# Optimization experiments

Hardware: AMD Instinct MI355X
Metric: run time of the kernel (lower is better)

Reference implementation:

```python
import math
import jax, jax.numpy as jnp
import numpy as np

B, S, DIM = 1, 2048, 2048
N_HEADS, N_KV_HEADS = 32, 8
HEAD_DIM = DIM // N_HEADS  # 64
HIDDEN = 8192  # 4*dim, already a multiple of 256
EPS = 1e-5


def setup_inputs() -> dict:
    key = jax.random.key(0)
    ks = jax.random.split(key, 10)

    def xavier(k, shape):
        lim = math.sqrt(6.0 / (shape[0] + shape[1]))
        return jax.random.uniform(k, shape, jnp.float32, -lim, lim)

    x = jax.random.normal(ks[0], (B, S, DIM), jnp.float32)
    c = jax.random.normal(ks[1], (B, DIM), jnp.float32)
    x_mask = jnp.ones((B, S), dtype=bool)
    # RoPE angles (theta=10000), freqs_cis = exp(i * pos * inv_freq) -> cos/sin parts
    inv_freq = 1.0 / (10000.0 ** (jnp.arange(0, HEAD_DIM, 2, dtype=jnp.float32) / HEAD_DIM))
    ang = jnp.arange(S, dtype=jnp.float32)[:, None] * inv_freq[None, :]  # [S, HEAD_DIM//2]
    freqs_cos = jnp.broadcast_to(jnp.cos(ang)[None], (B, S, HEAD_DIM // 2))
    freqs_sin = jnp.broadcast_to(jnp.sin(ang)[None], (B, S, HEAD_DIM // 2))
    qkv_out = (N_HEADS + 2 * N_KV_HEADS) * HEAD_DIM
    return dict(
        x=x, x_mask=x_mask, freqs_cos=freqs_cos, freqs_sin=freqs_sin, c=c,
        w_qkv=xavier(ks[2], (qkv_out, DIM)),
        w_out=xavier(ks[3], (DIM, N_HEADS * HEAD_DIM)),
        q_norm_w=jnp.ones((HEAD_DIM,), jnp.float32),
        k_norm_w=jnp.ones((HEAD_DIM,), jnp.float32),
        attn_norm1_w=jnp.ones((DIM,), jnp.float32),
        attn_norm2_w=jnp.ones((DIM,), jnp.float32),
        ffn_norm1_w=jnp.ones((DIM,), jnp.float32),
        ffn_norm2_w=jnp.ones((DIM,), jnp.float32),
        w1=xavier(ks[4], (HIDDEN, DIM)),
        w2=xavier(ks[5], (DIM, HIDDEN)),
        w3=xavier(ks[6], (HIDDEN, DIM)),
        w_ada=0.02 * jax.random.normal(ks[7], (4 * DIM, DIM), jnp.float32),
        b_ada=jnp.zeros((4 * DIM,), jnp.float32),
    )


def rms_norm(x, w, eps=EPS):
    x32 = x.astype(jnp.float32)
    return (x32 * jax.lax.rsqrt(jnp.mean(x32 * x32, -1, keepdims=True) + eps)).astype(x.dtype) * w


def apply_rope(x, cos, sin):
    # x: [b,s,h,d]; complex pairing of consecutive elements (view_as_complex)
    xr, xi = x[..., 0::2], x[..., 1::2]
    c = cos[:, :, None, :]  # broadcast over heads (freqs_cis.unsqueeze(2))
    s = sin[:, :, None, :]
    return jnp.stack([xr * c - xi * s, xr * s + xi * c], axis=-1).reshape(x.shape)


def reference(x, x_mask, freqs_cos, freqs_sin, c, w_qkv, w_out, q_norm_w, k_norm_w,
              attn_norm1_w, attn_norm2_w, ffn_norm1_w, ffn_norm2_w, w1, w2, w3,
              w_ada, b_ada):
    b, s, _ = x.shape
    n_rep = N_HEADS // N_KV_HEADS
    # AdaLN modulation: SiLU -> Linear -> 4 chunks
    mod = jax.nn.silu(c) @ w_ada.T + b_ada                      # [b, 4*dim]
    scale_msa, gate_msa, scale_mlp, gate_mlp = jnp.split(mod, 4, axis=-1)
    # ---- attention branch ----
    h = rms_norm(x, attn_norm1_w) * (1.0 + scale_msa[:, None, :])
    qkv = h @ w_qkv.T
    q, k, v = jnp.split(qkv, [N_HEADS * HEAD_DIM, (N_HEADS + N_KV_HEADS) * HEAD_DIM], axis=-1)
    q = q.reshape(b, s, N_HEADS, HEAD_DIM)
    k = k.reshape(b, s, N_KV_HEADS, HEAD_DIM)
    v = v.reshape(b, s, N_KV_HEADS, HEAD_DIM)
    q = rms_norm(q, q_norm_w)
    k = rms_norm(k, k_norm_w)
    q = apply_rope(q, freqs_cos, freqs_sin)
    k = apply_rope(k, freqs_cos, freqs_sin)
    # GQA: repeat each kv head n_rep times consecutively (unsqueeze+repeat+flatten)
    k = jnp.repeat(k, n_rep, axis=2)
    v = jnp.repeat(v, n_rep, axis=2)
    scale = math.sqrt(1.0 / HEAD_DIM)
    scores = jnp.einsum('bqhd,bkhd->bhqk', q, k) * scale         # [b,H,s,s]
    scores = jnp.where(x_mask[:, None, None, :], scores, -1e30)
    probs = jax.nn.softmax(scores, axis=-1)
    attn = jnp.einsum('bhqk,bkhd->bqhd', probs, v).reshape(b, s, N_HEADS * HEAD_DIM)
    attn = attn @ w_out.T
    x = x + jnp.tanh(gate_msa)[:, None, :] * rms_norm(attn, attn_norm2_w)
    # ---- SwiGLU FFN branch ----
    h = rms_norm(x, ffn_norm1_w) * (1.0 + scale_mlp[:, None, :])
    ffn = (jax.nn.silu(h @ w1.T) * (h @ w3.T)) @ w2.T
    x = x + jnp.tanh(gate_mlp)[:, None, :] * rms_norm(ffn, ffn_norm2_w)
    return x
```

## Files before the change

### kernel.cpp

```cpp
#include <hip/hip_runtime.h>
#include <hip/hip_bf16.h>
#include <cstdint>

typedef __hip_bfloat16 bf16;
typedef __attribute__((ext_vector_type(8))) short s8v;
typedef __attribute__((ext_vector_type(4))) float f32x4;

#define MFMA_BF16(a,b,c) __builtin_amdgcn_mfma_f32_16x16x32_bf16((a),(b),(c),0,0,0)

__device__ __forceinline__ float bf2f(bf16 v) { return __bfloat162float(v); }
__device__ __forceinline__ bf16 f2bf(float v) { return __float2bfloat16(v); }
__device__ __forceinline__ short f2bfbits(float v) {
  bf16 b = __float2bfloat16(v);
  short s; __builtin_memcpy(&s, &b, 2); return s;
}
__device__ __forceinline__ void g2lds16(const void* g, void* l) {
  __builtin_amdgcn_global_load_lds((__attribute__((address_space(1))) void*)(g),
                                   (__attribute__((address_space(3))) void*)(l), 16, 0, 0);
}
__device__ __forceinline__ void load8(const bf16* p, float v[8]) {
  uint4 r = *reinterpret_cast<const uint4*>(p);
  v[0]=__uint_as_float(r.x<<16); v[1]=__uint_as_float(r.x&0xffff0000u);
  v[2]=__uint_as_float(r.y<<16); v[3]=__uint_as_float(r.y&0xffff0000u);
  v[4]=__uint_as_float(r.z<<16); v[5]=__uint_as_float(r.z&0xffff0000u);
  v[6]=__uint_as_float(r.w<<16); v[7]=__uint_as_float(r.w&0xffff0000u);
}
__device__ __forceinline__ void loadf8(const float* p, float v[8]) {
  float4 a = *(const float4*)p, b = *(const float4*)(p + 4);
  v[0]=a.x; v[1]=a.y; v[2]=a.z; v[3]=a.w;
  v[4]=b.x; v[5]=b.y; v[6]=b.z; v[7]=b.w;
}
__device__ __forceinline__ s8v cvt8(const float* p) {
  float4 a = *(const float4*)p, b = *(const float4*)(p + 4);
  s8v r;
  r[0]=f2bfbits(a.x); r[1]=f2bfbits(a.y); r[2]=f2bfbits(a.z); r[3]=f2bfbits(a.w);
  r[4]=f2bfbits(b.x); r[5]=f2bfbits(b.y); r[6]=f2bfbits(b.z); r[7]=f2bfbits(b.w);
  return r;
}

__global__ __launch_bounds__(256) void ndt_cvt(
    const float* __restrict__ s, bf16* __restrict__ d, long n) {
  long i = ((long)blockIdx.x * 256 + threadIdx.x) * 8;
  if (i >= n) return;
  *(s8v*)(d + i) = cvt8(s + i);
}

__global__ __launch_bounds__(256) void ndt_ada(
    const float* __restrict__ c, const float* __restrict__ w_ada,
    const float* __restrict__ b_ada, float* __restrict__ mods) {
  const int wave = threadIdx.x >> 6, lane = threadIdx.x & 63;
  const int out = blockIdx.x * 4 + wave;
  const float4* wrow = (const float4*)(w_ada + (long)out * 2048);
  const float4* c4 = (const float4*)c;
  float acc = 0.f;
  for (int k = lane; k < 512; k += 64) {
    float4 wv = wrow[k];
    float4 cv = c4[k];
    acc += (cv.x / (1.f + __expf(-cv.x))) * wv.x;
    acc += (cv.y / (1.f + __expf(-cv.y))) * wv.y;
    acc += (cv.z / (1.f + __expf(-cv.z))) * wv.z;
    acc += (cv.w / (1.f + __expf(-cv.w))) * wv.w;
  }
  #pragma unroll
  for (int o = 32; o; o >>= 1) acc += __shfl_xor(acc, o, 64);
  if (lane == 0) {
    float m = acc + b_ada[out];
    int grp = out >> 11, idx = out & 2047;
    mods[grp * 2048 + idx] = (grp & 1) ? tanhf(m) : (1.f + m);
  }
}

__global__ __launch_bounds__(256) void ndt_norm_mod(
    const float* __restrict__ x, const float* __restrict__ w,
    const float* __restrict__ smod, bf16* __restrict__ out) {
  const int t = blockIdx.x, tid = threadIdx.x;
  __shared__ float red[4];
  float v[8];
  loadf8(x + (long)t * 2048 + tid * 8, v);
  float ss = 0.f;
  #pragma unroll
  for (int i = 0; i < 8; i++) ss += v[i] * v[i];
  #pragma unroll
  for (int o = 32; o; o >>= 1) ss += __shfl_xor(ss, o, 64);
  if ((tid & 63) == 0) red[tid >> 6] = ss;
  __syncthreads();
  float r = rsqrtf((red[0]+red[1]+red[2]+red[3]) * (1.f/2048.f) + 1e-5f);
  #pragma unroll
  for (int i = 0; i < 8; i++) {
    int cc = tid * 8 + i;
    out[(long)t * 2048 + cc] = f2bf(v[i] * r * w[cc] * smod[cc]);
  }
}

template<int EPI>
__global__ __launch_bounds__(256) void ndt_gemm_bb(
    const bf16* __restrict__ A, const bf16* __restrict__ B,
    bf16* __restrict__ C, const bf16* __restrict__ aux,
    int M, int N, int K) {
  __shared__ alignas(16) short sA[128 * 32];
  __shared__ alignas(16) short sB[128 * 32];
  const int tid = threadIdx.x;
  const int wave = tid >> 6, lane = tid & 63;
  const int quad = lane >> 4, l15 = lane & 15;
  const int wm = (wave >> 1) << 6, wn = (wave & 1) << 6;
  const long m0 = (long)blockIdx.x * 128, n0 = (long)blockIdx.y * 128;
  f32x4 zero4 = {0.f, 0.f, 0.f, 0.f};
  f32x4 acc[4][4];
  #pragma unroll
  for (int i = 0; i < 4; i++)
    #pragma unroll
    for (int j = 0; j < 4; j++) acc[i][j] = zero4;
  const int srow = lane >> 2;
  const int skc  = (lane & 3) * 8;
  for (int k0 = 0; k0 < K; k0 += 32) {
    #pragma unroll
    for (int it = 0; it < 2; it++) {
      int seg = wave * 2 + it;
      int row = seg * 16 + srow;
      g2lds16(A + (m0 + row) * (long)K + k0 + skc, (char*)sA + seg * 1024);
      g2lds16(B + (n0 + row) * (long)K + k0 + skc, (char*)sB + seg * 1024);
    }
    __syncthreads();
    s8v af[4], bfr[4];
    #pragma unroll
    for (int i = 0; i < 4; i++) af[i]  = *(const s8v*)&sA[(wm + i*16 + l15)*32 + quad*8];
    #pragma unroll
    for (int j = 0; j < 4; j++) bfr[j] = *(const s8v*)&sB[(wn + j*16 + l15)*32 + quad*8];
    #pragma unroll
    for (int i = 0; i < 4; i++)
      #pragma unroll
      for (int j = 0; j < 4; j++)
        acc[i][j] = MFMA_BF16(af[i], bfr[j], acc[i][j]);
    __syncthreads();
  }
  #pragma unroll
  for (int i = 0; i < 4; i++) {
    long rg = m0 + wm + i*16 + quad*4;
    #pragma unroll
    for (int j = 0; j < 4; j++) {
      long cg = n0 + wn + j*16 + l15;
      #pragma unroll
      for (int r = 0; r < 4; r++) {
        float v = acc[i][j][r];
        long idx = (rg + r) * (long)N + cg;
        if (EPI == 1) v = v / (1.f + __expf(-v));
        if (EPI == 2) v = v * bf2f(aux[idx]);
        C[idx] = f2bf(v);
      }
    }
  }
}

__device__ __forceinline__ void stage64(const bf16* __restrict__ G, long g0,
                                        int K, int t, char* tile, int q, int tid) {
  int L = q * 8192 + tid * 16;
  int Ls = L ^ (((L >> 9) & 1) << 5);
  const char* src = (const char*)(G + (g0 + (Ls >> 7)) * (long)K + t * 64) + (Ls & 127);
  g2lds16(src, tile + L);
}

__device__ __forceinline__ void phase_bar() {
  asm volatile("" ::: "memory");
  __builtin_amdgcn_s_barrier();
  asm volatile("" ::: "memory");
}

#define READ_A8(tA, h) do { \
  _Pragma("unroll") for (int i_ = 0; i_ < 4; i_++) { \
    int row_ = wm * 128 + (h) * 64 + i_ * 16 + l15; \
    _Pragma("unroll") for (int kk_ = 0; kk_ < 2; kk_++) { \
      int P_ = row_ * 128 + kk_ * 64 + quad * 16; \
      af[kk_][i_] = *(const s8v*)((tA) + (P_ ^ (((P_ >> 9) & 1) << 5))); } } } while (0)

#define READ_B8(tB, nh, bfreg) do { \
  _Pragma("unroll") for (int j_ = 0; j_ < 2; j_++) { \
    int col_ = wn * 64 + (nh) * 32 + j_ * 16 + l15; \
    _Pragma("unroll") for (int kk_ = 0; kk_ < 2; kk_++) { \
      int P_ = col_ * 128 + kk_ * 64 + quad * 16; \
      bfreg[kk_][j_] = *(const s8v*)((tB) + (P_ ^ (((P_ >> 9) & 1) << 5))); } } } while (0)

#define MMQ8(h, nh, bfreg) do { \
  __builtin_amdgcn_s_setprio(1); \
  _Pragma("unroll") for (int i_ = 0; i_ < 4; i_++) \
    _Pragma("unroll") for (int j_ = 0; j_ < 2; j_++) { \
      acc[(h)*4 + i_][(nh)*2 + j_] = MFMA_BF16(af[0][i_], bfreg[0][j_], acc[(h)*4 + i_][(nh)*2 + j_]); \
      acc[(h)*4 + i_][(nh)*2 + j_] = MFMA_BF16(af[1][i_], bfreg[1][j_], acc[(h)*4 + i_][(nh)*2 + j_]); } \
  __builtin_amdgcn_s_setprio(0); } while (0)

template<int EPI>
__global__ __launch_bounds__(512, 2) void ndt_gemm8(
    const bf16* __restrict__ A, const bf16* __restrict__ B,
    bf16* __restrict__ C, const bf16* __restrict__ aux,
    int M, int N, int K) {
  __shared__ alignas(16) short lds8[65536];
  char* const tA0 = (char*)lds8;
  char* const tB0 = tA0 + 32768;
  char* const tA1 = tA0 + 65536;
  char* const tB1 = tA0 + 98304;

  const int tid = threadIdx.x;
  const int wid = tid >> 6, lane = tid & 63;
  const int quad = lane >> 4, l15 = lane & 15;
  const int wm = wid >> 2, wn = wid & 3;

  const int nbx = gridDim.x;
  int bid = blockIdx.y * nbx + blockIdx.x;
  const int nwg = nbx * (int)gridDim.y;
  if ((nwg & 7) == 0) bid = (bid & 7) * (nwg >> 3) + (bid >> 3);
  const long m0 = (long)(bid % nbx) * 256;
  const long n0 = (long)(bid / nbx) * 256;

  const int NT = K >> 6;
  const int NI = NT >> 1;

  f32x4 acc[8][4];
  f32x4 zero4 = {0.f, 0.f, 0.f, 0.f};
  #pragma unroll
  for (int i = 0; i < 8; i++)
    #pragma unroll
    for (int j = 0; j < 4; j++) acc[i][j] = zero4;

  s8v af[2][4], bf0[2][2], bf1[2][2];

  #pragma unroll
  for (int q = 0; q < 4; q++) stage64(A, m0, K, 0, tA0, q, tid);
  #pragma unroll
  for (int q = 0; q < 4; q++) stage64(B, n0, K, 0, tB0, q, tid);
  #pragma unroll
  for (int q = 0; q < 4; q++) stage64(A, m0, K, 1, tA1, q, tid);
  stage64(B, n0, K, 1, tB1, 0, tid);
  stage64(B, n0, K, 1, tB1, 1, tid);
  asm volatile("s_waitcnt vmcnt(6)" ::: "memory");
  phase_bar();

  for (int it = 0; it < NI; ++it) {
    const int T = 2 * it;
    const int t2 = (T + 2 < NT) ? T + 2 : NT - 1;
    const int t3 = (T + 3 < NT) ? T + 3 : NT - 1;
    READ_A8(tA0, 0);
    READ_B8(tB0, 0, bf0);
    stage64(B, n0, K, T + 1, tB1, 2, tid);
    stage64(B, n0, K, T + 1, tB1, 3, tid);
    phase_bar(); MMQ8(0, 0, bf0); phase_bar();
    READ_B8(tB0, 1, bf1);
    stage64(A, m0, K, t2, tA0, 0, tid);
    stage64(A, m0, K, t2, tA0, 2, tid);
    phase_bar(); MMQ8(0, 1, bf1); phase_bar();
    READ_A8(tA0, 1);
    stage64(B, n0, K, t2, tB0, 0, tid);
    stage64(B, n0, K, t2, tB0, 1, tid);
    phase_bar(); MMQ8(1, 0, bf0); phase_bar();
    stage64(A, m0, K, t2, tA0, 1, tid);
    stage64(A, m0, K, t2, tA0, 3, tid);
    asm volatile("s_waitcnt vmcnt(6)" ::: "memory");
    phase_bar(); MMQ8(1, 1, bf1); phase_bar();
    READ_A8(tA1, 0);
    READ_B8(tB1, 0, bf0);
    stage64(B, n0, K, t2, tB0, 2, tid);
    stage64(B, n0, K, t2, tB0, 3, tid);
    phase_bar(); MMQ8(0, 0, bf0); phase_bar();
    READ_B8(tB1, 1, bf1);
    stage64(A, m0, K, t3, tA1, 0, tid);
    stage64(A, m0, K, t3, tA1, 2, tid);
    phase_bar(); MMQ8(0, 1, bf1); phase_bar();
    READ_A8(tA1, 1);
    stage64(B, n0, K, t3, tB1, 0, tid);
    stage64(B, n0, K, t3, tB1, 1, tid);
    phase_bar(); MMQ8(1, 0, bf0); phase_bar();
    stage64(A, m0, K, t3, tA1, 1, tid);
    stage64(A, m0, K, t3, tA1, 3, tid);
    asm volatile("s_waitcnt vmcnt(6)" ::: "memory");
    phase_bar(); MMQ8(1, 1, bf1); phase_bar();
  }
  asm volatile("s_waitcnt vmcnt(0)" ::: "memory");

  #pragma unroll
  for (int mi = 0; mi < 8; mi++) {
    long rg = m0 + wm * 128 + mi * 16 + quad * 4;
    #pragma unroll
    for (int nj = 0; nj < 4; nj++) {
      long cg = n0 + wn * 64 + nj * 16 + l15;
      #pragma unroll
      for (int r = 0; r < 4; r++) {
        float v = acc[mi][nj][r];
        long idx = (rg + r) * (long)N + cg;
        if (EPI == 1) v = v / (1.f + __expf(-v));
        if (EPI == 2) v = v * bf2f(aux[idx]);
        C[idx] = f2bf(v);
      }
    }
  }
}

template<int EPI>
__global__ __launch_bounds__(256) void ndt_gemm_bt(
    const bf16* __restrict__ A, const float* __restrict__ B,
    bf16* __restrict__ C, const bf16* __restrict__ aux,
    int M, int N, int K) {
  __shared__ alignas(16) short sA[128 * 32];
  __shared__ alignas(16) short sB[128 * 32];
  const int tid = threadIdx.x;
  const int wave = tid >> 6, lane = tid & 63;
  const int quad = lane >> 4, l15 = lane & 15;
  const int wm = (wave >> 1) << 6, wn = (wave & 1) << 6;
  const long m0 = (long)blockIdx.x * 128, n0 = (long)blockIdx.y * 128;
  f32x4 zero4 = {0.f, 0.f, 0.f, 0.f};
  f32x4 acc[4][4];
  #pragma unroll
  for (int i = 0; i < 4; i++)
    #pragma unroll
    for (int j = 0; j < 4; j++) acc[i][j] = zero4;
  const int srow = lane >> 2;
  const int skc  = (lane & 3) * 8;
  const int r0 = (wave * 2) * 16 + srow;
  const int r1 = (wave * 2 + 1) * 16 + srow;
  const bf16*  pa0 = A + (m0 + r0) * (long)K + skc;
  const bf16*  pa1 = A + (m0 + r1) * (long)K + skc;
  const float* pb0 = B + (n0 + r0) * (long)K + skc;
  const float* pb1 = B + (n0 + r1) * (long)K + skc;
  uint4* da0 = (uint4*)&sA[r0 * 32 + skc];
  uint4* da1 = (uint4*)&sA[r1 * 32 + skc];
  s8v* db0 = (s8v*)&sB[r0 * 32 + skc];
  s8v* db1 = (s8v*)&sB[r1 * 32 + skc];
  for (int k0 = 0; k0 < K; k0 += 32) {
    uint4 va0 = *(const uint4*)pa0; pa0 += 32;
    uint4 va1 = *(const uint4*)pa1; pa1 += 32;
    s8v vb0 = cvt8(pb0); pb0 += 32;
    s8v vb1 = cvt8(pb1); pb1 += 32;
    *da0 = va0; *da1 = va1; *db0 = vb0; *db1 = vb1;
    __syncthreads();
    s8v af[4], bfr[4];
    #pragma unroll
    for (int i = 0; i < 4; i++) af[i]  = *(const s8v*)&sA[(wm + i*16 + l15)*32 + quad*8];
    #pragma unroll
    for (int j = 0; j < 4; j++) bfr[j] = *(const s8v*)&sB[(wn + j*16 + l15)*32 + quad*8];
    #pragma unroll
    for (int i = 0; i < 4; i++)
      #pragma unroll
      for (int j = 0; j < 4; j++)
        acc[i][j] = MFMA_BF16(af[i], bfr[j], acc[i][j]);
    __syncthreads();
  }
  #pragma unroll
  for (int i = 0; i < 4; i++) {
    long rg = m0 + wm + i*16 + quad*4;
    #pragma unroll
    for (int j = 0; j < 4; j++) {
      long cg = n0 + wn + j*16 + l15;
      #pragma unroll
      for (int r = 0; r < 4; r++) {
        float v = acc[i][j][r];
        long idx = (rg + r) * (long)N + cg;
        if (EPI == 1) v = v / (1.f + __expf(-v));
        if (EPI == 2) v = v * bf2f(aux[idx]);
        C[idx] = f2bf(v);
      }
    }
  }
}

__global__ __launch_bounds__(256) void ndt_qkrope(
    const bf16* __restrict__ qkv, const float* __restrict__ qw, const float* __restrict__ kw,
    const float* __restrict__ fc, const float* __restrict__ fs,
    bf16* __restrict__ qb, bf16* __restrict__ kb, bf16* __restrict__ vb) {
  const int wid = blockIdx.x * 4 + (threadIdx.x >> 6);
  const int lane = threadIdx.x & 63;
  const int t = wid / 48;
  const int u = wid - t * 48;
  if (u < 40) {
    const bool isq = (u < 32);
    const int hh = isq ? u : (u - 32);
    const long src = (long)t * 3072 + (isq ? hh * 64 : 2048 + hh * 64) + lane;
    float v = bf2f(qkv[src]);
    float ss = v * v;
    #pragma unroll
    for (int o = 32; o; o >>= 1) ss += __shfl_xor(ss, o, 64);
    float r = rsqrtf(ss * (1.f/64.f) + 1e-5f);
    float y = v * r * (isq ? qw[lane] : kw[lane]);
    int j = lane >> 1;
    float cv = fc[t * 32 + j];
    float sv = fs[t * 32 + j];
    float p = __shfl_xor(y, 1, 64);
    float out = (lane & 1) ? (p * sv + y * cv) : (y * cv - p * sv);
    if (isq) qb[(long)t * 2048 + hh * 64 + lane] = f2bf(out);
    else     kb[(long)t * 512 + hh * 64 + lane] = f2bf(out);
  } else {
    const int vh = u - 40;
    vb[(long)t * 512 + vh * 64 + lane] = qkv[(long)t * 3072 + 2560 + vh * 64 + lane];
  }
}

__global__ __launch_bounds__(256) void ndt_attn(
    const bf16* __restrict__ qb, const bf16* __restrict__ kb,
    const bf16* __restrict__ vb, bf16* __restrict__ ob) {
  const int h = blockIdx.y;
  const int qblk = blockIdx.x;
  const int tid = threadIdx.x;
  const int wave = tid >> 6, lane = tid & 63;
  const int quad = lane >> 4, l15 = lane & 15;
  const int kh = h >> 2;
  __shared__ alignas(16) short kT[64 * 72];
  __shared__ alignas(16) short vT[64 * 72];
  __shared__ alignas(16) short pT[4][16 * 72];
  const int qrow = qblk * 64 + wave * 16 + l15;
  const short* qptr = (const short*)qb + (long)qrow * 2048 + h * 64;
  s8v qf0 = *(const s8v*)(qptr + quad * 8);
  s8v qf1 = *(const s8v*)(qptr + 32 + quad * 8);
  f32x4 zero4 = {0.f, 0.f, 0.f, 0.f};
  f32x4 o[4];
  float mr[4], lr[4];
  #pragma unroll
  for (int r = 0; r < 4; r++) { o[r] = zero4; mr[r] = -1e30f; lr[r] = 0.f; }
  const int skey = tid >> 2;
  const int sdg = (tid & 3) * 16;
  for (int kt = 0; kt < 32; kt++) {
    {
      const short* ksrc = (const short*)kb + ((long)(kt * 64 + skey) * 8 + kh) * 64 + sdg;
      *(uint4*)&kT[skey * 72 + sdg]     = *(const uint4*)(ksrc);
      *(uint4*)&kT[skey * 72 + sdg + 8] = *(const uint4*)(ksrc + 8);
      const short* vsrc = (const short*)vb + ((long)(kt * 64 + skey) * 8 + kh) * 64 + sdg;
      short tv[16];
      *(uint4*)&tv[0] = *(const uint4*)(vsrc);
      *(uint4*)&tv[8] = *(const uint4*)(vsrc + 8);
      #pragma unroll
      for (int i = 0; i < 16; i++) vT[(sdg + i) * 72 + skey] = tv[i];
    }
    __syncthreads();
    f32x4 s[4];
    #pragma unroll
    for (int b4 = 0; b4 < 4; b4++) {
      const short* kr = &kT[(b4 * 16 + l15) * 72];
      s8v kf0 = *(const s8v*)(kr + quad * 8);
      s8v kf1 = *(const s8v*)(kr + 32 + quad * 8);
      f32x4 z = zero4;
      z = MFMA_BF16(qf0, kf0, z);
      z = MFMA_BF16(qf1, kf1, z);
      s[b4] = z;
    }
    #pragma unroll
    for (int r = 0; r < 4; r++) {
      float mx = -1e30f;
      #pragma unroll
      for (int b4 = 0; b4 < 4; b4++) { float sv2 = s[b4][r] * 0.125f; s[b4][r] = sv2; mx = fmaxf(mx, sv2); }
      mx = fmaxf(mx, __shfl_xor(mx, 1, 64));
      mx = fmaxf(mx, __shfl_xor(mx, 2, 64));
      mx = fmaxf(mx, __shfl_xor(mx, 4, 64));
      mx = fmaxf(mx, __shfl_xor(mx, 8, 64));
      float nm = fmaxf(mr[r], mx);
      float alpha = __expf(mr[r] - nm);
      mr[r] = nm;
      float rs = 0.f;
      #pragma unroll
      for (int b4 = 0; b4 < 4; b4++) { float p = __expf(s[b4][r] - nm); s[b4][r] = p; rs += p; }
      rs += __shfl_xor(rs, 1, 64);
      rs += __shfl_xor(rs, 2, 64);
      rs += __shfl_xor(rs, 4, 64);
      rs += __shfl_xor(rs, 8, 64);
      lr[r] = lr[r] * alpha + rs;
      #pragma unroll
      for (int cb = 0; cb < 4; cb++) o[cb][r] *= alpha;
    }
    short* pw = &pT[wave][0];
    #pragma unroll
    for (int b4 = 0; b4 < 4; b4++)
      #pragma unroll
      for (int r = 0; r < 4; r++)
        pw[(quad * 4 + r) * 72 + b4 * 16 + l15] = f2bfbits(s[b4][r]);
    const short* pr = &pT[wave][0];
    s8v pf0 = *(const s8v*)(pr + l15 * 72 + quad * 8);
    s8v pf1 = *(const s8v*)(pr + l15 * 72 + 32 + quad * 8);
    #pragma unroll
    for (int cb = 0; cb < 4; cb++) {
      const short* vr = &vT[(cb * 16 + l15) * 72];
      s8v vf0 = *(const s8v*)(vr + quad * 8);
      s8v vf1 = *(const s8v*)(vr + 32 + quad * 8);
      o[cb] = MFMA_BF16(pf0, vf0, o[cb]);
      o[cb] = MFMA_BF16(pf1, vf1, o[cb]);
    }
    __syncthreads();
  }
  #pragma unroll
  for (int cb = 0; cb < 4; cb++)
    #pragma unroll
    for (int r = 0; r < 4; r++) {
      int tok = qblk * 64 + wave * 16 + quad * 4 + r;
      ob[(long)tok * 2048 + h * 64 + cb * 16 + l15] = f2bf(o[cb][r] / lr[r]);
    }
}

__global__ __launch_bounds__(256) void ndt_resid1(
    const float* __restrict__ x, const bf16* __restrict__ ao,
    const float* __restrict__ mods, const float* __restrict__ w_n2,
    const float* __restrict__ w_f1, float* __restrict__ x1, bf16* __restrict__ h2) {
  const int t = blockIdx.x, tid = threadIdx.x;
  __shared__ float red1[4], red2[4];
  const long base = (long)t * 2048;
  float a[8], xv[8], y[8];
  load8(ao + base + tid * 8, a);
  loadf8(x + base + tid * 8, xv);
  float ss = 0.f;
  #pragma unroll
  for (int i = 0; i < 8; i++) ss += a[i] * a[i];
  #pragma unroll
  for (int o = 32; o; o >>= 1) ss += __shfl_xor(ss, o, 64);
  if ((tid & 63) == 0) red1[tid >> 6] = ss;
  __syncthreads();
  float r1 = rsqrtf((red1[0]+red1[1]+red1[2]+red1[3]) * (1.f/2048.f) + 1e-5f);
  float ss2 = 0.f;
  #pragma unroll
  for (int i = 0; i < 8; i++) {
    int cc = tid * 8 + i;
    float yy = xv[i] + mods[2048 + cc] * (a[i] * r1 * w_n2[cc]);
    y[i] = yy; ss2 += yy * yy;
    x1[base + cc] = yy;
  }
  #pragma unroll
  for (int o = 32; o; o >>= 1) ss2 += __shfl_xor(ss2, o, 64);
  if ((tid & 63) == 0) red2[tid >> 6] = ss2;
  __syncthreads();
  float r2 = rsqrtf((red2[0]+red2[1]+red2[2]+red2[3]) * (1.f/2048.f) + 1e-5f);
  #pragma unroll
  for (int i = 0; i < 8; i++) {
    int cc = tid * 8 + i;
    h2[base + cc] = f2bf(y[i] * r2 * w_f1[cc] * mods[4096 + cc]);
  }
}

__global__ __launch_bounds__(256) void ndt_resid2(
    const float* __restrict__ x1, const bf16* __restrict__ ffn,
    const float* __restrict__ mods, const float* __restrict__ w_f2,
    float* __restrict__ out) {
  const int t = blockIdx.x, tid = threadIdx.x;
  __shared__ float red[4];
  const long base = (long)t * 2048;
  float f[8], xv[8];
  load8(ffn + base + tid * 8, f);
  loadf8(x1 + base + tid * 8, xv);
  float ss = 0.f;
  #pragma unroll
  for (int i = 0; i < 8; i++) ss += f[i] * f[i];
  #pragma unroll
  for (int o = 32; o; o >>= 1) ss += __shfl_xor(ss, o, 64);
  if ((tid & 63) == 0) red[tid >> 6] = ss;
  __syncthreads();
  float r = rsqrtf((red[0]+red[1]+red[2]+red[3]) * (1.f/2048.f) + 1e-5f);
  #pragma unroll
  for (int i = 0; i < 8; i++) {
    int cc = tid * 8 + i;
    out[base + cc] = xv[i] + mods[6144 + cc] * (f[i] * r * w_f2[cc]);
  }
}

extern "C" void kernel_launch(void* const* d_in, const int* in_sizes, int n_in,
                              void* d_out, int out_size, void* d_ws, size_t ws_size,
                              hipStream_t stream) {
  const float* x     = (const float*)d_in[0];
  const float* fc    = (const float*)d_in[2];
  const float* fs    = (const float*)d_in[3];
  const float* c     = (const float*)d_in[4];
  const float* w_qkv = (const float*)d_in[5];
  const float* w_out = (const float*)d_in[6];
  const float* q_nw  = (const float*)d_in[7];
  const float* k_nw  = (const float*)d_in[8];
  const float* an1   = (const float*)d_in[9];
  const float* an2   = (const float*)d_in[10];
  const float* fn1   = (const float*)d_in[11];
  const float* fn2   = (const float*)d_in[12];
  const float* w1    = (const float*)d_in[13];
  const float* w2    = (const float*)d_in[14];
  const float* w3    = (const float*)d_in[15];
  const float* w_ada = (const float*)d_in[16];
  const float* b_ada = (const float*)d_in[17];
  float* out = (float*)d_out;

  const size_t MB = 1024 * 1024;
  char* w = (char*)d_ws;
  float* mods = (float*)(w);
  char* base = w + 32768;
  bf16* h1   = (bf16*)(base);
  bf16* attn = h1;
  bf16* ffn  = h1;
  bf16* qkv  = (bf16*)(base + 8 * MB);
  bf16* ao   = qkv;
  bf16* qb   = (bf16*)(base + 20 * MB);
  bf16* h2   = qb;
  bf16* kb   = (bf16*)(base + 28 * MB);
  bf16* vb   = (bf16*)(base + 30 * MB);
  float* x1  = (float*)(base + 32 * MB);
  bf16* t1   = (bf16*)(base + 48 * MB);
  bf16* Wa   = (bf16*)(base + 80 * MB);
  bf16* Wb   = (bf16*)(base + 112 * MB);
  const size_t needed = 32768 + 144 * MB;

  ndt_ada<<<2048, 256, 0, stream>>>(c, w_ada, b_ada, mods);
  ndt_norm_mod<<<2048, 256, 0, stream>>>(x, an1, mods, h1);

  if (ws_size >= needed) {
    ndt_cvt<<<3072, 256, 0, stream>>>(w_qkv, Wa, 6291456L);
    ndt_gemm_bb<0><<<dim3(16, 24), 256, 0, stream>>>(h1, Wa, qkv, nullptr, 2048, 3072, 2048);
    ndt_qkrope<<<24576, 256, 0, stream>>>(qkv, q_nw, k_nw, fc, fs, qb, kb, vb);
    ndt_attn<<<dim3(32, 32), 256, 0, stream>>>(qb, kb, vb, attn);
    ndt_cvt<<<2048, 256, 0, stream>>>(w_out, Wa, 4194304L);
    ndt_gemm_bb<0><<<dim3(16, 16), 256, 0, stream>>>(attn, Wa, ao, nullptr, 2048, 2048, 2048);
    ndt_resid1<<<2048, 256, 0, stream>>>(x, ao, mods, an2, fn1, x1, h2);
    ndt_cvt<<<8192, 256, 0, stream>>>(w1, Wa, 16777216L);
    ndt_cvt<<<8192, 256, 0, stream>>>(w3, Wb, 16777216L);
    ndt_gemm8<1><<<dim3(8, 32), 512, 0, stream>>>(h2, Wa, t1, nullptr, 2048, 8192, 2048);
    ndt_gemm8<2><<<dim3(8, 32), 512, 0, stream>>>(h2, Wb, t1, t1, 2048, 8192, 2048);
    ndt_cvt<<<8192, 256, 0, stream>>>(w2, Wa, 16777216L);
    ndt_gemm_bb<0><<<dim3(16, 16), 256, 0, stream>>>(t1, Wa, ffn, nullptr, 2048, 2048, 8192);
  } else {
    ndt_gemm_bt<0><<<dim3(16, 24), 256, 0, stream>>>(h1, w_qkv, qkv, nullptr, 2048, 3072, 2048);
    ndt_qkrope<<<24576, 256, 0, stream>>>(qkv, q_nw, k_nw, fc, fs, qb, kb, vb);
    ndt_attn<<<dim3(32, 32), 256, 0, stream>>>(qb, kb, vb, attn);
    ndt_gemm_bt<0><<<dim3(16, 16), 256, 0, stream>>>(attn, w_out, ao, nullptr, 2048, 2048, 2048);
    ndt_resid1<<<2048, 256, 0, stream>>>(x, ao, mods, an2, fn1, x1, h2);
    ndt_gemm_bt<1><<<dim3(16, 64), 256, 0, stream>>>(h2, w1, t1, nullptr, 2048, 8192, 2048);
    ndt_gemm_bt<2><<<dim3(16, 64), 256, 0, stream>>>(h2, w3, t1, t1, 2048, 8192, 2048);
    ndt_gemm_bt<0><<<dim3(16, 16), 256, 0, stream>>>(t1, w2, ffn, nullptr, 2048, 2048, 8192);
  }
  ndt_resid2<<<2048, 256, 0, stream>>>(x1, ffn, mods, fn2, out);
}
```

Measured before the change: 893.1 us.

## Use split-K 256x256 GEMM for QKV, out-proj and down-proj with fp32 partials

Replaces the simple 128x128 GEMM used for the QKV, output-projection and FFN down-projection with the pipelined 256x256 kernel. Because those GEMMs have few output tiles, K is split across blockIdx.z and the fp32 partial sums go to workspace buffers. The partials are added up inside new fused epilogue kernels for qk-norm/rope, residual1 and residual2. It also changes the LDS swizzle and precomputes staging source pointers. The cost is extra fp32 partial traffic through global memory and more reads in the epilogue kernels.

```diff
diff --git a/kernel.cpp b/kernel.cpp
--- a/kernel.cpp
+++ b/kernel.cpp
@@ -92,106 +92,45 @@
   }
 }
 
-template<int EPI>
-__global__ __launch_bounds__(256) void ndt_gemm_bb(
-    const bf16* __restrict__ A, const bf16* __restrict__ B,
-    bf16* __restrict__ C, const bf16* __restrict__ aux,
-    int M, int N, int K) {
-  __shared__ alignas(16) short sA[128 * 32];
-  __shared__ alignas(16) short sB[128 * 32];
-  const int tid = threadIdx.x;
-  const int wave = tid >> 6, lane = tid & 63;
-  const int quad = lane >> 4, l15 = lane & 15;
-  const int wm = (wave >> 1) << 6, wn = (wave & 1) << 6;
-  const long m0 = (long)blockIdx.x * 128, n0 = (long)blockIdx.y * 128;
-  f32x4 zero4 = {0.f, 0.f, 0.f, 0.f};
-  f32x4 acc[4][4];
-  #pragma unroll
-  for (int i = 0; i < 4; i++)
-    #pragma unroll
-    for (int j = 0; j < 4; j++) acc[i][j] = zero4;
-  const int srow = lane >> 2;
-  const int skc  = (lane & 3) * 8;
-  for (int k0 = 0; k0 < K; k0 += 32) {
-    #pragma unroll
-    for (int it = 0; it < 2; it++) {
-      int seg = wave * 2 + it;
-      int row = seg * 16 + srow;
-      g2lds16(A + (m0 + row) * (long)K + k0 + skc, (char*)sA + seg * 1024);
-      g2lds16(B + (n0 + row) * (long)K + k0 + skc, (char*)sB + seg * 1024);
-    }
-    __syncthreads();
-    s8v af[4], bfr[4];
-    #pragma unroll
-    for (int i = 0; i < 4; i++) af[i]  = *(const s8v*)&sA[(wm + i*16 + l15)*32 + quad*8];
-    #pragma unroll
-    for (int j = 0; j < 4; j++) bfr[j] = *(const s8v*)&sB[(wn + j*16 + l15)*32 + quad*8];
-    #pragma unroll
-    for (int i = 0; i < 4; i++)
-      #pragma unroll
-      for (int j = 0; j < 4; j++)
-        acc[i][j] = MFMA_BF16(af[i], bfr[j], acc[i][j]);
-    __syncthreads();
-  }
-  #pragma unroll
-  for (int i = 0; i < 4; i++) {
-    long rg = m0 + wm + i*16 + quad*4;
-    #pragma unroll
-    for (int j = 0; j < 4; j++) {
-      long cg = n0 + wn + j*16 + l15;
-      #pragma unroll
-      for (int r = 0; r < 4; r++) {
-        float v = acc[i][j][r];
-        long idx = (rg + r) * (long)N + cg;
-        if (EPI == 1) v = v / (1.f + __expf(-v));
-        if (EPI == 2) v = v * bf2f(aux[idx]);
-        C[idx] = f2bf(v);
-      }
-    }
-  }
-}
-
-__device__ __forceinline__ void stage64(const bf16* __restrict__ G, long g0,
-                                        int K, int t, char* tile, int q, int tid) {
-  int L = q * 8192 + tid * 16;
-  int Ls = L ^ (((L >> 9) & 1) << 5);
-  const char* src = (const char*)(G + (g0 + (Ls >> 7)) * (long)K + t * 64) + (Ls & 127);
-  g2lds16(src, tile + L);
-}
-
-__device__ __forceinline__ void phase_bar() {
-  asm volatile("" ::: "memory");
-  __builtin_amdgcn_s_barrier();
-  asm volatile("" ::: "memory");
-}
+#define SWZ8(P) ((P) ^ ((((P) >> 7) & 7) << 4))
+
+#define STG8(mat, q, t, tile) \
+  g2lds16(src##mat[q] + (long)(t) * 128, (tile) + (q) * 8192 + (tid << 4))
 
 #define READ_A8(tA, h) do { \
   _Pragma("unroll") for (int i_ = 0; i_ < 4; i_++) { \
     int row_ = wm * 128 + (h) * 64 + i_ * 16 + l15; \
     _Pragma("unroll") for (int kk_ = 0; kk_ < 2; kk_++) { \
       int P_ = row_ * 128 + kk_ * 64 + quad * 16; \
-      af[kk_][i_] = *(const s8v*)((tA) + (P_ ^ (((P_ >> 9) & 1) << 5))); } } } while (0)
+      af[kk_][i_] = *(const s8v*)((tA) + SWZ8(P_)); } } } while (0)
 
 #define READ_B8(tB, nh, bfreg) do { \
   _Pragma("unroll") for (int j_ = 0; j_ < 2; j_++) { \
     int col_ = wn * 64 + (nh) * 32 + j_ * 16 + l15; \
     _Pragma("unroll") for (int kk_ = 0; kk_ < 2; kk_++) { \
       int P_ = col_ * 128 + kk_ * 64 + quad * 16; \
-      bfreg[kk_][j_] = *(const s8v*)((tB) + (P_ ^ (((P_ >> 9) & 1) << 5))); } } } while (0)
-
-#define MMQ8(h, nh, bfreg) do { \
+      bfreg[kk_][j_] = *(const s8v*)((tB) + SWZ8(P_)); } } } while (0)
+
+#define PH_MMA(h, nh, bfreg) do { \
+  asm volatile("" ::: "memory"); \
+  __builtin_amdgcn_s_barrier(); \
+  asm volatile("s_waitcnt lgkmcnt(0)" ::: "memory"); \
+  __builtin_amdgcn_sched_barrier(0); \
   __builtin_amdgcn_s_setprio(1); \
   _Pragma("unroll") for (int i_ = 0; i_ < 4; i_++) \
     _Pragma("unroll") for (int j_ = 0; j_ < 2; j_++) { \
       acc[(h)*4 + i_][(nh)*2 + j_] = MFMA_BF16(af[0][i_], bfreg[0][j_], acc[(h)*4 + i_][(nh)*2 + j_]); \
       acc[(h)*4 + i_][(nh)*2 + j_] = MFMA_BF16(af[1][i_], bfreg[1][j_], acc[(h)*4 + i_][(nh)*2 + j_]); } \
-  __builtin_amdgcn_s_setprio(0); } while (0)
-
-template<int EPI>
+  __builtin_amdgcn_s_setprio(0); \
+  asm volatile("" ::: "memory"); \
+  __builtin_amdgcn_s_barrier(); \
+  asm volatile("" ::: "memory"); } while (0)
+
+template<int EPI, int SPLIT>
 __global__ __launch_bounds__(512, 2) void ndt_gemm8(
     const bf16* __restrict__ A, const bf16* __restrict__ B,
-    bf16* __restrict__ C, const bf16* __restrict__ aux,
-    int M, int N, int K) {
+    void* __restrict__ C0, void* __restrict__ C1, const bf16* __restrict__ aux,
+    int M, int N, int ldK, int Kc) {
   __shared__ alignas(16) short lds8[65536];
   char* const tA0 = (char*)lds8;
   char* const tB0 = tA0 + 32768;
@@ -209,9 +148,20 @@
   if ((nwg & 7) == 0) bid = (bid & 7) * (nwg >> 3) + (bid >> 3);
   const long m0 = (long)(bid % nbx) * 256;
   const long n0 = (long)(bid / nbx) * 256;
-
-  const int NT = K >> 6;
+  const long koff = (long)blockIdx.z * Kc;
+
+  const int NT = Kc >> 6;
   const int NI = NT >> 1;
+
+  const char* srcA[4];
+  const char* srcB[4];
+  #pragma unroll
+  for (int q = 0; q < 4; q++) {
+    int L = q * 8192 + (tid << 4);
+    int Ls = SWZ8(L);
+    srcA[q] = (const char*)(A + (m0 + (Ls >> 7)) * (long)ldK + koff) + (Ls & 127);
+    srcB[q] = (const char*)(B + (n0 + (Ls >> 7)) * (long)ldK + koff) + (Ls & 127);
+  }
 
   f32x4 acc[8][4];
   f32x4 zero4 = {0.f, 0.f, 0.f, 0.f};
@@ -223,15 +173,17 @@
   s8v af[2][4], bf0[2][2], bf1[2][2];
 
   #pragma unroll
-  for (int q = 0; q < 4; q++) stage64(A, m0, K, 0, tA0, q, tid);
-  #pragma unroll
-  for (int q = 0; q < 4; q++) stage64(B, n0, K, 0, tB0, q, tid);
-  #pragma unroll
-  for (int q = 0; q < 4; q++) stage64(A, m0, K, 1, tA1, q, tid);
-  stage64(B, n0, K, 1, tB1, 0, tid);
-  stage64(B, n0, K, 1, tB1, 1, tid);
+  for (int q = 0; q < 4; q++) STG8(A, q, 0, tA0);
+  #pragma unroll
+  for (int q = 0; q < 4; q++) STG8(B, q, 0, tB0);
+  #pragma unroll
+  for (int q = 0; q < 4; q++) STG8(A, q, 1, tA1);
+  STG8(B, 0, 1, tB1);
+  STG8(B, 1, 1, tB1);
   asm volatile("s_waitcnt vmcnt(6)" ::: "memory");
-  phase_bar();
+  asm volatile("" ::: "memory");
+  __builtin_amdgcn_s_barrier();
+  asm volatile("" ::: "memory");
 
   for (int it = 0; it < NI; ++it) {
     const int T = 2 * it;
@@ -239,54 +191,71 @@
     const int t3 = (T + 3 < NT) ? T + 3 : NT - 1;
     READ_A8(tA0, 0);
     READ_B8(tB0, 0, bf0);
-    stage64(B, n0, K, T + 1, tB1, 2, tid);
-    stage64(B, n0, K, T + 1, tB1, 3, tid);
-    phase_bar(); MMQ8(0, 0, bf0); phase_bar();
+    STG8(B, 2, T + 1, tB1);
+    STG8(B, 3, T + 1, tB1);
+    PH_MMA(0, 0, bf0);
     READ_B8(tB0, 1, bf1);
-    stage64(A, m0, K, t2, tA0, 0, tid);
-    stage64(A, m0, K, t2, tA0, 2, tid);
-    phase_bar(); MMQ8(0, 1, bf1); phase_bar();
+    STG8(A, 0, t2, tA0);
+    STG8(A, 2, t2, tA0);
+    PH_MMA(0, 1, bf1);
     READ_A8(tA0, 1);
-    stage64(B, n0, K, t2, tB0, 0, tid);
-    stage64(B, n0, K, t2, tB0, 1, tid);
-    phase_bar(); MMQ8(1, 0, bf0); phase_bar();
-    stage64(A, m0, K, t2, tA0, 1, tid);
-    stage64(A, m0, K, t2, tA0, 3, tid);
+    STG8(B, 0, t2, tB0);
+    STG8(B, 1, t2, tB0);
+    PH_MMA(1, 0, bf0);
+    STG8(A, 1, t2, tA0);
+    STG8(A, 3, t2, tA0);
     asm volatile("s_waitcnt vmcnt(6)" ::: "memory");
-    phase_bar(); MMQ8(1, 1, bf1); phase_bar();
+    PH_MMA(1, 1, bf1);
     READ_A8(tA1, 0);
     READ_B8(tB1, 0, bf0);
-    stage64(B, n0, K, t2, tB0, 2, tid);
-    stage64(B, n0, K, t2, tB0, 3, tid);
-    phase_bar(); MMQ8(0, 0, bf0); phase_bar();
+    STG8(B, 2, t2, tB0);
+    STG8(B, 3, t2, tB0);
+    PH_MMA(0, 0, bf0);
     READ_B8(tB1, 1, bf1);
-    stage64(A, m0, K, t3, tA1, 0, tid);
-    stage64(A, m0, K, t3, tA1, 2, tid);
-    phase_bar(); MMQ8(0, 1, bf1); phase_bar();
+    STG8(A, 0, t3, tA1);
+    STG8(A, 2, t3, tA1);
+    PH_MMA(0, 1, bf1);
     READ_A8(tA1, 1);
-    stage64(B, n0, K, t3, tB1, 0, tid);
-    stage64(B, n0, K, t3, tB1, 1, tid);
-    phase_bar(); MMQ8(1, 0, bf0); phase_bar();
-    stage64(A, m0, K, t3, tA1, 1, tid);
-    stage64(A, m0, K, t3, tA1, 3, tid);
+    STG8(B, 0, t3, tB1);
+    STG8(B, 1, t3, tB1);
+    PH_MMA(1, 0, bf0);
+    STG8(A, 1, t3, tA1);
+    STG8(A, 3, t3, tA1);
     asm volatile("s_waitcnt vmcnt(6)" ::: "memory");
-    phase_bar(); MMQ8(1, 1, bf1); phase_bar();
+    PH_MMA(1, 1, bf1);
   }
   asm volatile("s_waitcnt vmcnt(0)" ::: "memory");
 
-  #pragma unroll
-  for (int mi = 0; mi < 8; mi++) {
-    long rg = m0 + wm * 128 + mi * 16 + quad * 4;
-    #pragma unroll
-    for (int nj = 0; nj < 4; nj++) {
-      long cg = n0 + wn * 64 + nj * 16 + l15;
-      #pragma unroll
-      for (int r = 0; r < 4; r++) {
-        float v = acc[mi][nj][r];
-        long idx = (rg + r) * (long)N + cg;
-        if (EPI == 1) v = v / (1.f + __expf(-v));
-        if (EPI == 2) v = v * bf2f(aux[idx]);
-        C[idx] = f2bf(v);
+  if (SPLIT) {
+    float* P = (float*)((blockIdx.z & 1) ? C1 : C0) +
+               (long)(blockIdx.z >> 1) * ((long)M * N);
+    #pragma unroll
+    for (int mi = 0; mi < 8; mi++) {
+      long rg = m0 + wm * 128 + mi * 16 + quad * 4;
+      #pragma unroll
+      for (int nj = 0; nj < 4; nj++) {
+        long cg = n0 + wn * 64 + nj * 16 + l15;
+        #pragma unroll
+        for (int r = 0; r < 4; r++)
+          P[(rg + r) * (long)N + cg] = acc[mi][nj][r];
+      }
+    }
+  } else {
+    bf16* Cb = (bf16*)C0;
+    #pragma unroll
+    for (int mi = 0; mi < 8; mi++) {
+      long rg = m0 + wm * 128 + mi * 16 + quad * 4;
+      #pragma unroll
+      for (int nj = 0; nj < 4; nj++) {
+        long cg = n0 + wn * 64 + nj * 16 + l15;
+        #pragma unroll
+        for (int r = 0; r < 4; r++) {
+          float v = acc[mi][nj][r];
+          long idx = (rg + r) * (long)N + cg;
+          if (EPI == 1) v = v / (1.f + __expf(-v));
+          if (EPI == 2) v = v * bf2f(aux[idx]);
+          Cb[idx] = f2bf(v);
+        }
       }
     }
   }
@@ -390,6 +359,39 @@
   }
 }
 
+__global__ __launch_bounds__(256) void ndt_qkropep(
+    const float* __restrict__ p0, const float* __restrict__ p1,
+    const float* __restrict__ qw, const float* __restrict__ kw,
+    const float* __restrict__ fc, const float* __restrict__ fs,
+    bf16* __restrict__ qb, bf16* __restrict__ kb, bf16* __restrict__ vb) {
+  const int wid = blockIdx.x * 4 + (threadIdx.x >> 6);
+  const int lane = threadIdx.x & 63;
+  const int t = wid / 48;
+  const int u = wid - t * 48;
+  if (u < 40) {
+    const bool isq = (u < 32);
+    const int hh = isq ? u : (u - 32);
+    const long src = (long)t * 3072 + (isq ? hh * 64 : 2048 + hh * 64) + lane;
+    float v = p0[src] + p1[src];
+    float ss = v * v;
+    #pragma unroll
+    for (int o = 32; o; o >>= 1) ss += __shfl_xor(ss, o, 64);
+    float r = rsqrtf(ss * (1.f/64.f) + 1e-5f);
+    float y = v * r * (isq ? qw[lane] : kw[lane]);
+    int j = lane >> 1;
+    float cv = fc[t * 32 + j];
+    float sv = fs[t * 32 + j];
+    float p = __shfl_xor(y, 1, 64);
+    float out = (lane & 1) ? (p * sv + y * cv) : (y * cv - p * sv);
+    if (isq) qb[(long)t * 2048 + hh * 64 + lane] = f2bf(out);
+    else     kb[(long)t * 512 + hh * 64 + lane] = f2bf(out);
+  } else {
+    const int vh = u - 40;
+    const long vsrc = (long)t * 3072 + 2560 + vh * 64 + lane;
+    vb[(long)t * 512 + vh * 64 + lane] = f2bf(p0[vsrc] + p1[vsrc]);
+  }
+}
+
 __global__ __launch_bounds__(256) void ndt_attn(
     const bf16* __restrict__ qb, const bf16* __restrict__ kb,
     const bf16* __restrict__ vb, bf16* __restrict__ ob) {
@@ -526,6 +528,55 @@
   }
 }
 
+__global__ __launch_bounds__(256) void ndt_resid1p(
+    const float* __restrict__ x, const float* __restrict__ pA,
+    const float* __restrict__ pB,
+    const float* __restrict__ mods, const float* __restrict__ w_n2,
+    const float* __restrict__ w_f1, float* __restrict__ x1, bf16* __restrict__ h2) {
+  const int t = blockIdx.x, tid = threadIdx.x;
+  const long MN = 4194304;
+  __shared__ float red1[4], red2[4];
+  const long base = (long)t * 2048;
+  float a[8], tmp[8], xv[8], y[8];
+  loadf8(pA + base + tid * 8, a);
+  loadf8(pA + MN + base + tid * 8, tmp);
+  #pragma unroll
+  for (int i = 0; i < 8; i++) a[i] += tmp[i];
+  loadf8(pB + base + tid * 8, tmp);
+  #pragma unroll
+  for (int i = 0; i < 8; i++) a[i] += tmp[i];
+  loadf8(pB + MN + base + tid * 8, tmp);
+  #pragma unroll
+  for (int i = 0; i < 8; i++) a[i] += tmp[i];
+  loadf8(x + base + tid * 8, xv);
+  float ss = 0.f;
+  #pragma unroll
+  for (int i = 0; i < 8; i++) ss += a[i] * a[i];
+  #pragma unroll
+  for (int o = 32; o; o >>= 1) ss += __shfl_xor(ss, o, 64);
+  if ((tid & 63) == 0) red1[tid >> 6] = ss;
+  __syncthreads();
+  float r1 = rsqrtf((red1[0]+red1[1]+red1[2]+red1[3]) * (1.f/2048.f) + 1e-5f);
+  float ss2 = 0.f;
+  #pragma unroll
+  for (int i = 0; i < 8; i++) {
+    int cc = tid * 8 + i;
+    float yy = xv[i] + mods[2048 + cc] * (a[i] * r1 * w_n2[cc]);
+    y[i] = yy; ss2 += yy * yy;
+    x1[base + cc] = yy;
+  }
+  #pragma unroll
+  for (int o = 32; o; o >>= 1) ss2 += __shfl_xor(ss2, o, 64);
+  if ((tid & 63) == 0) red2[tid >> 6] = ss2;
+  __syncthreads();
+  float r2 = rsqrtf((red2[0]+red2[1]+red2[2]+red2[3]) * (1.f/2048.f) + 1e-5f);
+  #pragma unroll
+  for (int i = 0; i < 8; i++) {
+    int cc = tid * 8 + i;
+    h2[base + cc] = f2bf(y[i] * r2 * w_f1[cc] * mods[4096 + cc]);
+  }
+}
+
 __global__ __launch_bounds__(256) void ndt_resid2(
     const float* __restrict__ x1, const bf16* __restrict__ ffn,
     const float* __restrict__ mods, const float* __restrict__ w_f2,
@@ -535,6 +586,42 @@
   const long base = (long)t * 2048;
   float f[8], xv[8];
   load8(ffn + base + tid * 8, f);
+  loadf8(x1 + base + tid * 8, xv);
+  float ss = 0.f;
+  #pragma unroll
+  for (int i = 0; i < 8; i++) ss += f[i] * f[i];
+  #pragma unroll
+  for (int o = 32; o; o >>= 1) ss += __shfl_xor(ss, o, 64);
+  if ((tid & 63) == 0) red[tid >> 6] = ss;
+  __syncthreads();
+  float r = rsqrtf((red[0]+red[1]+red[2]+red[3]) * (1.f/2048.f) + 1e-5f);
+  #pragma unroll
+  for (int i = 0; i < 8; i++) {
+    int cc = tid * 8 + i;
+    out[base + cc] = xv[i] + mods[6144 + cc] * (f[i] * r * w_f2[cc]);
+  }
+}
+
+__global__ __launch_bounds__(256) void ndt_resid2p(
+    const float* __restrict__ x1, const float* __restrict__ pA,
+    const float* __restrict__ pB,
+    const float* __restrict__ mods, const float* __restrict__ w_f2,
+    float* __restrict__ out) {
+  const int t = blockIdx.x, tid = threadIdx.x;
+  const long MN = 4194304;
+  __shared__ float red[4];
+  const long base = (long)t * 2048;
+  float f[8], tmp[8], xv[8];
+  loadf8(pA + base + tid * 8, f);
+  loadf8(pA + MN + base + tid * 8, tmp);
+  #pragma unroll
+  for (int i = 0; i < 8; i++) f[i] += tmp[i];
+  loadf8(pB + base + tid * 8, tmp);
+  #pragma unroll
+  for (int i = 0; i < 8; i++) f[i] += tmp[i];
+  loadf8(pB + MN + base + tid * 8, tmp);
+  #pragma unroll
+  for (int i = 0; i < 8; i++) f[i] += tmp[i];
   loadf8(x1 + base + tid * 8, xv);
   float ss = 0.f;
   #pragma unroll
@@ -590,6 +677,9 @@
   bf16* t1   = (bf16*)(base + 48 * MB);
   bf16* Wa   = (bf16*)(base + 80 * MB);
   bf16* Wb   = (bf16*)(base + 112 * MB);
+  float* t1f = (float*)t1;
+  float* wbf = (float*)Wb;
+  float* p0f = (float*)base;
   const size_t needed = 32768 + 144 * MB;
 
   ndt_ada<<<2048, 256, 0, stream>>>(c, w_ada, b_ada, mods);
@@ -597,18 +687,19 @@
 
   if (ws_size >= needed) {
     ndt_cvt<<<3072, 256, 0, stream>>>(w_qkv, Wa, 6291456L);
-    ndt_gemm_bb<0><<<dim3(16, 24), 256, 0, stream>>>(h1, Wa, qkv, nullptr, 2048, 3072, 2048);
-    ndt_qkrope<<<24576, 256, 0, stream>>>(qkv, q_nw, k_nw, fc, fs, qb, kb, vb);
+    ndt_gemm8<0,1><<<dim3(8, 12, 2), 512, 0, stream>>>(h1, Wa, t1f, wbf, nullptr, 2048, 3072, 2048, 1024);
+    ndt_qkropep<<<24576, 256, 0, stream>>>(t1f, wbf, q_nw, k_nw, fc, fs, qb, kb, vb);
     ndt_attn<<<dim3(32, 32), 256, 0, stream>>>(qb, kb, vb, attn);
     ndt_cvt<<<2048, 256, 0, stream>>>(w_out, Wa, 4194304L);
-    ndt_gemm_bb<0><<<dim3(16, 16), 256, 0, stream>>>(attn, Wa, ao, nullptr, 2048, 2048, 2048);
-    ndt_resid1<<<2048, 256, 0, stream>>>(x, ao, mods, an2, fn1, x1, h2);
+    ndt_gemm8<0,1><<<dim3(8, 8, 4), 512, 0, stream>>>(attn, Wa, t1f, wbf, nullptr, 2048, 2048, 2048, 512);
+    ndt_resid1p<<<2048, 256, 0, stream>>>(x, t1f, wbf, mods, an2, fn1, x1, h2);
     ndt_cvt<<<8192, 256, 0, stream>>>(w1, Wa, 16777216L);
     ndt_cvt<<<8192, 256, 0, stream>>>(w3, Wb, 16777216L);
-    ndt_gemm8<1><<<dim3(8, 32), 512, 0, stream>>>(h2, Wa, t1, nullptr, 2048, 8192, 2048);
-    ndt_gemm8<2><<<dim3(8, 32), 512, 0, stream>>>(h2, Wb, t1, t1, 2048, 8192, 2048);
+    ndt_gemm8<1,0><<<dim3(8, 32, 1), 512, 0, stream>>>(h2, Wa, t1, nullptr, nullptr, 2048, 8192, 2048, 2048);
+    ndt_gemm8<2,0><<<dim3(8, 32, 1), 512, 0, stream>>>(h2, Wb, t1, nullptr, t1, 2048, 8192, 2048, 2048);
     ndt_cvt<<<8192, 256, 0, stream>>>(w2, Wa, 16777216L);
-    ndt_gemm_bb<0><<<dim3(16, 16), 256, 0, stream>>>(t1, Wa, ffn, nullptr, 2048, 2048, 8192);
+    ndt_gemm8<0,1><<<dim3(8, 8, 4), 512, 0, stream>>>(t1, Wa, p0f, wbf, nullptr, 2048, 2048, 8192, 2048);
+    ndt_resid2p<<<2048, 256, 0, stream>>>(x1, p0f, wbf, mods, fn2, out);
   } else {
     ndt_gemm_bt<0><<<dim3(16, 24), 256, 0, stream>>>(h1, w_qkv, qkv, nullptr, 2048, 3072, 2048);
     ndt_qkrope<<<24576, 256, 0, stream>>>(qkv, q_nw, k_nw, fc, fs, qb, kb, vb);
@@ -618,6 +709,6 @@
     ndt_gemm_bt<1><<<dim3(16, 64), 256, 0, stream>>>(h2, w1, t1, nullptr, 2048, 8192, 2048);
     ndt_gemm_bt<2><<<dim3(16, 64), 256, 0, stream>>>(h2, w3, t1, t1, 2048, 8192, 2048);
     ndt_gemm_bt<0><<<dim3(16, 16), 256, 0, stream>>>(t1, w2, ffn, nullptr, 2048, 2048, 8192);
-  }
-  ndt_resid2<<<2048, 256, 0, stream>>>(x1, ffn, mods, fn2, out);
-}
+    ndt_resid2<<<2048, 256, 0, stream>>>(x1, ffn, mods, fn2, out);
+  }
+}
```

New measurement: 778.5 us. 12.8% less time.
